# Kernel optimization log

Hardware: AMD Instinct MI355X
Metric: run time of the kernel (lower is better)

## Reference

```python
import jax, jax.numpy as jnp
import numpy as np

H = 4096
V = 32000
BT = 2048
IGNORE_INDEX = -100
WEIGHT_HARD = 0.5
WEIGHT_SOFT = 0.5
EPS = 1e-12  # F.normalize eps


def setup_inputs() -> dict:
    key = jax.random.key(0)
    k0, k1, k2, k3, k4 = jax.random.split(key, 5)
    student = jax.random.normal(k0, (BT, H // 2), dtype=jnp.float32)
    teacher = jax.random.normal(k1, (BT, H), dtype=jnp.float32)
    W_student = jax.random.normal(k2, (V, H // 2), dtype=jnp.float32) * (1.0 / np.sqrt(H // 2))
    W_teacher = jax.random.normal(k3, (V, H), dtype=jnp.float32) * (1.0 / np.sqrt(H))
    target = jax.random.randint(k4, (BT,), 0, V, dtype=jnp.int64)
    return {"student": student, "W_student": W_student, "teacher": teacher,
            "W_teacher": W_teacher, "target": target}


def reference(student, W_student, teacher, W_teacher, target):
    # Fused linear projections to vocab space
    s_logits = jnp.einsum("bh,vh->bv", student, W_student)   # [BT, V]
    t_logits = jnp.einsum("bh,vh->bv", teacher, W_teacher)   # [BT, V]

    n = target.shape[0]
    valid = target != IGNORE_INDEX                            # [BT]

    # Hard loss: cross-entropy(student_logits, target), sum over valid / BT
    logp = jax.nn.log_softmax(s_logits, axis=-1)
    safe_tgt = jnp.where(valid, target, 0)
    nll = -jnp.take_along_axis(logp, safe_tgt[:, None], axis=-1)[:, 0]
    hard_loss = jnp.sum(jnp.where(valid, nll, 0.0)) / n

    # Soft loss: 1 - cosine_similarity(student_logits, teacher_logits) per row
    s_norm = jnp.maximum(jnp.linalg.norm(s_logits, axis=-1, keepdims=True), EPS)
    t_norm = jnp.maximum(jnp.linalg.norm(t_logits, axis=-1, keepdims=True), EPS)
    cos = jnp.sum((s_logits / s_norm) * (t_logits / t_norm), axis=-1)  # [BT]
    soft_loss = jnp.sum(1.0 - cos) / n

    return WEIGHT_HARD * hard_loss + WEIGHT_SOFT * soft_loss
```

## Files before the change

kernel.cpp:

```cpp
#include <hip/hip_runtime.h>
#include <hip/hip_bf16.h>

#define H2 2048
#define HT 4096
#define NV 32000
#define NBT 2048

#define BM2 128
#define BN2 256
#define BK2 64
#define NVB2 (NV / BN2)

#define BM 128
#define BN 128
#define BK 32
#define LDT 40
#define NVB (NV / BN)

typedef __attribute__((ext_vector_type(8))) short short8;
typedef __attribute__((ext_vector_type(8))) unsigned short ushort8;
typedef __attribute__((ext_vector_type(4))) float floatx4;

static __device__ __forceinline__ unsigned int pk_bf16(float a, float b) {
  __hip_bfloat162 h = __float22bfloat162_rn(make_float2(a, b));
  union { __hip_bfloat162 h; unsigned int u; } c;
  c.h = h;
  return c.u;
}

static __device__ __forceinline__ void gload_lds16(const void* g, void* l) {
  __builtin_amdgcn_global_load_lds(
      (const __attribute__((address_space(1))) unsigned int*)g,
      (__attribute__((address_space(3))) unsigned int*)l, 16, 0, 0);
}

__global__ void cvt_bf16_kernel(const float* __restrict__ src,
                                unsigned int* __restrict__ dst, int n) {
  int i = blockIdx.x * blockDim.x + threadIdx.x;
  int base = i * 8;
  if (base >= n) return;
  float4 f0 = *(const float4*)(src + base);
  float4 f1 = *(const float4*)(src + base + 4);
  uint4 o;
  o.x = pk_bf16(f0.x, f0.y);
  o.y = pk_bf16(f0.z, f0.w);
  o.z = pk_bf16(f1.x, f1.y);
  o.w = pk_bf16(f1.z, f1.w);
  *(uint4*)(dst + i * 4) = o;
}


template <int K>
static __device__ __forceinline__ void gemm_pipe(
    const unsigned short* __restrict__ act,
    const unsigned short* __restrict__ w,
    const int row0, const int col0, const int tid,
    const int aoff, const int boff,
    unsigned short (*__restrict__ sA)[BM2 * BK2],
    unsigned short (*__restrict__ sB)[BN2 * BK2],
    floatx4 (&acc)[4][4])
{
  constexpr int NT = K / BK2;
  const int r8 = tid >> 3;
  const int usw = ((tid & 7) ^ (r8 & 7)) * 8;

  const unsigned short* pa0 = act + (size_t)(row0 + r8) * K + usw;
  const unsigned short* pa1 = pa0 + (size_t)64 * K;
  const unsigned short* pb0 = w + (size_t)(col0 + r8) * K + usw;
  const unsigned short* pb1 = pb0 + (size_t)64 * K;
  const unsigned short* pb2 = pb0 + (size_t)128 * K;
  const unsigned short* pb3 = pb0 + (size_t)192 * K;

#define STAGE6(buf)                                   \
  do {                                                \
    gload_lds16(pa0, &sA[buf][tid * 8]);              \
    gload_lds16(pa1, &sA[buf][4096 + tid * 8]);       \
    gload_lds16(pb0, &sB[buf][tid * 8]);              \
    gload_lds16(pb1, &sB[buf][4096 + tid * 8]);       \
    gload_lds16(pb2, &sB[buf][8192 + tid * 8]);       \
    gload_lds16(pb3, &sB[buf][12288 + tid * 8]);      \
    pa0 += BK2; pa1 += BK2;                           \
    pb0 += BK2; pb1 += BK2; pb2 += BK2; pb3 += BK2;   \
  } while (0)

  STAGE6(0);
  STAGE6(1);
  asm volatile("s_waitcnt vmcnt(6)" ::: "memory");
  __builtin_amdgcn_s_barrier();

#pragma unroll 1
  for (int t = 0; t < NT; ++t) {
    const int cur = t & 1;
    const unsigned short* sAc = sA[cur];
    const unsigned short* sBc = sB[cur];

    short8 a0[4], a1[4], b0[4], b1[4];
#pragma unroll
    for (int i = 0; i < 4; ++i) {
      a0[i] = *(const short8*)(sAc + (aoff + i * 1024));
      a1[i] = *(const short8*)(sAc + ((aoff ^ 32) + i * 1024));
    }
#pragma unroll
    for (int j = 0; j < 4; ++j) {
      b0[j] = *(const short8*)(sBc + (boff + j * 1024));
      b1[j] = *(const short8*)(sBc + ((boff ^ 32) + j * 1024));
    }
    asm volatile("s_waitcnt lgkmcnt(0)" ::: "memory");
    __builtin_amdgcn_s_barrier();

    if (t + 2 < NT) {
      STAGE6(cur);
      asm volatile("s_waitcnt vmcnt(6)" ::: "memory");
    } else if (t + 1 < NT) {
      asm volatile("s_waitcnt vmcnt(0)" ::: "memory");
    }
    __builtin_amdgcn_s_barrier();

    __builtin_amdgcn_s_setprio(1);
#pragma unroll
    for (int i = 0; i < 4; ++i)
#pragma unroll
      for (int j = 0; j < 4; ++j)
        acc[i][j] = __builtin_amdgcn_mfma_f32_16x16x32_bf16(
            a0[i], b0[j], acc[i][j], 0, 0, 0);
#pragma unroll
    for (int i = 0; i < 4; ++i)
#pragma unroll
      for (int j = 0; j < 4; ++j)
        acc[i][j] = __builtin_amdgcn_mfma_f32_16x16x32_bf16(
            a1[i], b1[j], acc[i][j], 0, 0, 0);
    __builtin_amdgcn_s_setprio(0);
  }
#undef STAGE6
}

__global__ __launch_bounds__(512, 2) void fused_gemm_pipe_kernel(
    const unsigned short* __restrict__ sbf,
    const unsigned short* __restrict__ tbf,
    const unsigned short* __restrict__ Wsb,
    const unsigned short* __restrict__ Wtb,
    const int* __restrict__ target,
    float* __restrict__ part,
    float* __restrict__ s_tgt_out)
{
  __shared__ unsigned short sA[2][BM2 * BK2];
  __shared__ unsigned short sB[2][BN2 * BK2];
  __shared__ float sRed[BM2][4];
  __shared__ int sTgt[BM2];

  const int tid = threadIdx.x;

  const int lin = blockIdx.x + (int)gridDim.x * blockIdx.y;
  const int swz = (lin & 7) * 250 + (lin >> 3);
  const int bx = swz & 15;
  const int by = swz >> 4;
  const int row0 = bx * BM2;
  const int col0 = by * BN2;

  if (tid < BM2) {
    sTgt[tid] = target[row0 + tid];
    sRed[tid][0] = 0.f; sRed[tid][1] = 0.f;
    sRed[tid][2] = 0.f; sRed[tid][3] = 0.f;
  }

  const int lane = tid & 63;
  const int wv = tid >> 6;
  const int wr = wv >> 2;
  const int wc = wv & 3;
  const int ku = lane >> 4;
  const int u0 = (ku ^ (lane & 7)) * 8;
  const int aoff = (wr * 64 + (lane & 15)) * BK2 + u0;
  const int boff = (wc * 64 + (lane & 15)) * BK2 + u0;

  floatx4 acc_s[4][4];
  floatx4 acc_t[4][4];
#pragma unroll
  for (int i = 0; i < 4; ++i)
#pragma unroll
    for (int j = 0; j < 4; ++j) {
      acc_s[i][j] = (floatx4){0.f, 0.f, 0.f, 0.f};
      acc_t[i][j] = (floatx4){0.f, 0.f, 0.f, 0.f};
    }

  gemm_pipe<H2>(sbf, Wsb, row0, col0, tid, aoff, boff, sA, sB, acc_s);
  gemm_pipe<HT>(tbf, Wtb, row0, col0, tid, aoff, boff, sA, sB, acc_t);

#pragma unroll
  for (int i = 0; i < 4; ++i) {
#pragma unroll
    for (int r = 0; r < 4; ++r) {
      const int row_l = wr * 64 + i * 16 + (lane >> 4) * 4 + r;
      float e = 0.f, dp = 0.f, ss = 0.f, tt = 0.f;
#pragma unroll
      for (int j = 0; j < 4; ++j) {
        float s = acc_s[i][j][r];
        float t = acc_t[i][j][r];
        e += __expf(s);
        dp += s * t;
        ss += s * s;
        tt += t * t;
        const int col_l = wc * 64 + j * 16 + (lane & 15);
        if (sTgt[row_l] == col0 + col_l) s_tgt_out[row0 + row_l] = s;
      }
#pragma unroll
      for (int off = 1; off < 16; off <<= 1) {
        e  += __shfl_xor(e,  off, 16);
        dp += __shfl_xor(dp, off, 16);
        ss += __shfl_xor(ss, off, 16);
        tt += __shfl_xor(tt, off, 16);
      }
      if ((lane & 15) == 0) {
        atomicAdd(&sRed[row_l][0], e);
        atomicAdd(&sRed[row_l][1], dp);
        atomicAdd(&sRed[row_l][2], ss);
        atomicAdd(&sRed[row_l][3], tt);
      }
    }
  }
  __syncthreads();
  if (tid < BM2) {
    float* p = part + (size_t)by * 4 * NBT + row0 + tid;
    p[0]       = sRed[tid][0];
    p[NBT]     = sRed[tid][1];
    p[2 * NBT] = sRed[tid][2];
    p[3 * NBT] = sRed[tid][3];
  }
}


__global__ __launch_bounds__(256, 2) void fused_gemm_kernel(
    const unsigned short* __restrict__ sbf,
    const unsigned short* __restrict__ tbf,
    const float* __restrict__ Ws,
    const float* __restrict__ Wt,
    const int* __restrict__ target,
    float* __restrict__ part,
    float* __restrict__ s_tgt_out)
{
  __shared__ unsigned short sA[BM * LDT];
  __shared__ unsigned short sB[BN * LDT];
  __shared__ float sRed[BM][4];
  __shared__ int sTgt[BM];

  const int tid = threadIdx.x;
  const int row0 = blockIdx.x * BM;
  const int col0 = blockIdx.y * BN;
  const int lane = tid & 63;
  const int wv = tid >> 6;
  const int wr = wv >> 1;
  const int wc = wv & 1;

  if (tid < BM) {
    sTgt[tid] = target[row0 + tid];
    sRed[tid][0] = 0.f; sRed[tid][1] = 0.f;
    sRed[tid][2] = 0.f; sRed[tid][3] = 0.f;
  }

  floatx4 acc_s[4][4];
  floatx4 acc_t[4][4];
#pragma unroll
  for (int i = 0; i < 4; ++i)
#pragma unroll
    for (int j = 0; j < 4; ++j) {
      acc_s[i][j] = (floatx4){0.f, 0.f, 0.f, 0.f};
      acc_t[i][j] = (floatx4){0.f, 0.f, 0.f, 0.f};
    }

  const int sr = tid >> 1;
  const int sk = (tid & 1) << 4;
  const int mrow = lane & 15;
  const int koff = (lane >> 4) << 3;
  const int abase = (wr * 64 + mrow) * LDT + koff;
  const int bbase = (wc * 64 + mrow) * LDT + koff;

  {
    const unsigned short* ap = sbf + (size_t)(row0 + sr) * H2 + sk;
    const float* bp = Ws + (size_t)(col0 + sr) * H2 + sk;
#pragma unroll 1
    for (int k0 = 0; k0 < H2; k0 += BK) {
      ushort8 a0 = *(const ushort8*)(ap);
      ushort8 a1 = *(const ushort8*)(ap + 8);
      float4 b0 = *(const float4*)(bp);
      float4 b1 = *(const float4*)(bp + 4);
      float4 b2 = *(const float4*)(bp + 8);
      float4 b3 = *(const float4*)(bp + 12);
      ap += BK; bp += BK;
      __syncthreads();
      *(ushort8*)(&sA[sr * LDT + sk]) = a0;
      *(ushort8*)(&sA[sr * LDT + sk + 8]) = a1;
      uint4 u0, u1;
      u0.x = pk_bf16(b0.x, b0.y); u0.y = pk_bf16(b0.z, b0.w);
      u0.z = pk_bf16(b1.x, b1.y); u0.w = pk_bf16(b1.z, b1.w);
      u1.x = pk_bf16(b2.x, b2.y); u1.y = pk_bf16(b2.z, b2.w);
      u1.z = pk_bf16(b3.x, b3.y); u1.w = pk_bf16(b3.z, b3.w);
      *(uint4*)(&sB[sr * LDT + sk]) = u0;
      *(uint4*)(&sB[sr * LDT + sk + 8]) = u1;
      __syncthreads();
      short8 af[4], bfrag[4];
#pragma unroll
      for (int i = 0; i < 4; ++i)
        af[i] = *(const short8*)(&sA[abase + i * 16 * LDT]);
#pragma unroll
      for (int j = 0; j < 4; ++j)
        bfrag[j] = *(const short8*)(&sB[bbase + j * 16 * LDT]);
#pragma unroll
      for (int i = 0; i < 4; ++i)
#pragma unroll
        for (int j = 0; j < 4; ++j)
          acc_s[i][j] = __builtin_amdgcn_mfma_f32_16x16x32_bf16(
              af[i], bfrag[j], acc_s[i][j], 0, 0, 0);
    }
  }
  {
    const unsigned short* ap = tbf + (size_t)(row0 + sr) * HT + sk;
    const float* bp = Wt + (size_t)(col0 + sr) * HT + sk;
#pragma unroll 1
    for (int k0 = 0; k0 < HT; k0 += BK) {
      ushort8 a0 = *(const ushort8*)(ap);
      ushort8 a1 = *(const ushort8*)(ap + 8);
      float4 b0 = *(const float4*)(bp);
      float4 b1 = *(const float4*)(bp + 4);
      float4 b2 = *(const float4*)(bp + 8);
      float4 b3 = *(const float4*)(bp + 12);
      ap += BK; bp += BK;
      __syncthreads();
      *(ushort8*)(&sA[sr * LDT + sk]) = a0;
      *(ushort8*)(&sA[sr * LDT + sk + 8]) = a1;
      uint4 u0, u1;
      u0.x = pk_bf16(b0.x, b0.y); u0.y = pk_bf16(b0.z, b0.w);
      u0.z = pk_bf16(b1.x, b1.y); u0.w = pk_bf16(b1.z, b1.w);
      u1.x = pk_bf16(b2.x, b2.y); u1.y = pk_bf16(b2.z, b2.w);
      u1.z = pk_bf16(b3.x, b3.y); u1.w = pk_bf16(b3.z, b3.w);
      *(uint4*)(&sB[sr * LDT + sk]) = u0;
      *(uint4*)(&sB[sr * LDT + sk + 8]) = u1;
      __syncthreads();
      short8 af[4], bfrag[4];
#pragma unroll
      for (int i = 0; i < 4; ++i)
        af[i] = *(const short8*)(&sA[abase + i * 16 * LDT]);
#pragma unroll
      for (int j = 0; j < 4; ++j)
        bfrag[j] = *(const short8*)(&sB[bbase + j * 16 * LDT]);
#pragma unroll
      for (int i = 0; i < 4; ++i)
#pragma unroll
        for (int j = 0; j < 4; ++j)
          acc_t[i][j] = __builtin_amdgcn_mfma_f32_16x16x32_bf16(
              af[i], bfrag[j], acc_t[i][j], 0, 0, 0);
    }
  }

#pragma unroll
  for (int i = 0; i < 4; ++i) {
#pragma unroll
    for (int r = 0; r < 4; ++r) {
      const int row_l = wr * 64 + i * 16 + (lane >> 4) * 4 + r;
      float e = 0.f, dp = 0.f, ss = 0.f, tt = 0.f;
#pragma unroll
      for (int j = 0; j < 4; ++j) {
        float s = acc_s[i][j][r];
        float t = acc_t[i][j][r];
        e += __expf(s);
        dp += s * t;
        ss += s * s;
        tt += t * t;
        const int col_l = wc * 64 + j * 16 + (lane & 15);
        if (sTgt[row_l] == col0 + col_l) s_tgt_out[row0 + row_l] = s;
      }
#pragma unroll
      for (int off = 1; off < 16; off <<= 1) {
        e  += __shfl_xor(e,  off, 16);
        dp += __shfl_xor(dp, off, 16);
        ss += __shfl_xor(ss, off, 16);
        tt += __shfl_xor(tt, off, 16);
      }
      if ((lane & 15) == 0) {
        atomicAdd(&sRed[row_l][0], e);
        atomicAdd(&sRed[row_l][1], dp);
        atomicAdd(&sRed[row_l][2], ss);
        atomicAdd(&sRed[row_l][3], tt);
      }
    }
  }
  __syncthreads();
  if (tid < BM) {
    float* p = part + (size_t)blockIdx.y * 4 * NBT + row0 + tid;
    p[0]       = sRed[tid][0];
    p[NBT]     = sRed[tid][1];
    p[2 * NBT] = sRed[tid][2];
    p[3 * NBT] = sRed[tid][3];
  }
}


__global__ void row_loss_kernel(const float* __restrict__ part,
                                const float* __restrict__ s_tgt,
                                const int* __restrict__ target,
                                float* __restrict__ row_loss, int nvb) {
  const int row = blockIdx.x * blockDim.x + threadIdx.x;
  if (row >= NBT) return;
  float e = 0.f, dp = 0.f, ss = 0.f, tt = 0.f;
  for (int v = 0; v < nvb; ++v) {
    const float* p = part + (size_t)v * 4 * NBT + row;
    e  += p[0];
    dp += p[NBT];
    ss += p[2 * NBT];
    tt += p[3 * NBT];
  }
  const float lse = logf(e);
  const int tg = target[row];
  const float st = s_tgt[row];
  const float nll = (tg != -100) ? (lse - st) : 0.f;
  const float ns = fmaxf(sqrtf(ss), 1e-12f);
  const float nt = fmaxf(sqrtf(tt), 1e-12f);
  const float c = dp / (ns * nt);
  row_loss[row] = (0.5f * nll + 0.5f * (1.f - c)) * (1.f / (float)NBT);
}

__global__ void final_reduce_kernel(const float* __restrict__ row_loss,
                                    float* __restrict__ out) {
  __shared__ float sm[4];
  float v = 0.f;
  for (int i = threadIdx.x; i < NBT; i += 256) v += row_loss[i];
#pragma unroll
  for (int off = 32; off >= 1; off >>= 1) v += __shfl_down(v, off, 64);
  if ((threadIdx.x & 63) == 0) sm[threadIdx.x >> 6] = v;
  __syncthreads();
  if (threadIdx.x == 0) out[0] = sm[0] + sm[1] + sm[2] + sm[3];
}

extern "C" void kernel_launch(void* const* d_in, const int* in_sizes, int n_in,
                              void* d_out, int out_size, void* d_ws, size_t ws_size,
                              hipStream_t stream) {
  const float* student = (const float*)d_in[0];
  const float* Ws      = (const float*)d_in[1];
  const float* teacher = (const float*)d_in[2];
  const float* Wt      = (const float*)d_in[3];
  const int*   target  = (const int*)d_in[4];

  const size_t nS  = (size_t)NBT * H2;
  const size_t nT  = (size_t)NBT * HT;
  const size_t nWs = (size_t)NV * H2;
  const size_t nWt = (size_t)NV * HT;
  const size_t nPart2 = (size_t)NVB2 * 4 * NBT;
  const size_t nPart  = (size_t)NVB * 4 * NBT;

  const size_t ws_needed_big =
      (nS + nT + nWs + nWt) * 2 + (nPart2 + 2 * NBT) * 4;

  if (ws_size >= ws_needed_big) {
    unsigned short* sbf = (unsigned short*)d_ws;
    unsigned short* tbf = sbf + nS;
    unsigned short* Wsb = tbf + nT;
    unsigned short* Wtb = Wsb + nWs;
    float* part     = (float*)(Wtb + nWt);
    float* s_tgt    = part + nPart2;
    float* row_loss = s_tgt + NBT;

    cvt_bf16_kernel<<<(int)(nS / 8 / 256), 256, 0, stream>>>(
        student, (unsigned int*)sbf, (int)nS);
    cvt_bf16_kernel<<<(int)(nT / 8 / 256), 256, 0, stream>>>(
        teacher, (unsigned int*)tbf, (int)nT);
    cvt_bf16_kernel<<<(int)(nWs / 8 / 256), 256, 0, stream>>>(
        Ws, (unsigned int*)Wsb, (int)nWs);
    cvt_bf16_kernel<<<(int)(nWt / 8 / 256), 256, 0, stream>>>(
        Wt, (unsigned int*)Wtb, (int)nWt);

    dim3 grid(NBT / BM2, NV / BN2);
    fused_gemm_pipe_kernel<<<grid, 512, 0, stream>>>(
        sbf, tbf, Wsb, Wtb, target, part, s_tgt);

    row_loss_kernel<<<NBT / 256, 256, 0, stream>>>(part, s_tgt, target,
                                                   row_loss, NVB2);
    final_reduce_kernel<<<1, 256, 0, stream>>>(row_loss, (float*)d_out);
  } else {
    unsigned short* sbf = (unsigned short*)d_ws;
    unsigned short* tbf = sbf + nS;
    float* part     = (float*)(tbf + nT);
    float* s_tgt    = part + nPart;
    float* row_loss = s_tgt + NBT;

    cvt_bf16_kernel<<<(int)(nS / 8 / 256), 256, 0, stream>>>(
        student, (unsigned int*)sbf, (int)nS);
    cvt_bf16_kernel<<<(int)(nT / 8 / 256), 256, 0, stream>>>(
        teacher, (unsigned int*)tbf, (int)nT);

    dim3 grid(NBT / BM, NV / BN);
    fused_gemm_kernel<<<grid, 256, 0, stream>>>(sbf, tbf, Ws, Wt, target,
                                                part, s_tgt);

    row_loss_kernel<<<NBT / 256, 256, 0, stream>>>(part, s_tgt, target,
                                                   row_loss, NVB);
    final_reduce_kernel<<<1, 256, 0, stream>>>(row_loss, (float*)d_out);
  }
}
```

Measured before the change: 1.986 ms.

## Triple-buffer GEMM LDS pipeline, merge bf16 conversions, wave-parallel row loss

The pipelined GEMM moves from double to triple LDS buffering. Loads for stage t+2 are issued before reading stage t, so one barrier pair per iteration covers the global-to-LDS latency. Launch bounds drop to one block per SM because the shared memory footprint grows. The four bf16 conversion launches are merged into one grid-stride kernel, and row_loss now has each 64-lane wave reduce one row's partials with shuffles instead of a serial loop per thread. The risk is that lower occupancy could offset the deeper pipeline.

```diff
diff --git a/kernel.cpp b/kernel.cpp
--- a/kernel.cpp
+++ b/kernel.cpp
@@ -49,6 +49,36 @@
   *(uint4*)(dst + i * 4) = o;
 }
 
+__global__ void cvt_all_kernel(const float* __restrict__ s0,
+                               const float* __restrict__ s1,
+                               const float* __restrict__ s2,
+                               const float* __restrict__ s3,
+                               unsigned int* __restrict__ d0,
+                               unsigned int* __restrict__ d1,
+                               unsigned int* __restrict__ d2,
+                               unsigned int* __restrict__ d3,
+                               int c0, int c1, int c2, int c3) {
+  for (int g = blockIdx.x * blockDim.x + threadIdx.x; g < c3;
+       g += gridDim.x * blockDim.x) {
+    const float* src;
+    unsigned int* dst;
+    int l;
+    if (g < c0)      { src = s0; dst = d0; l = g; }
+    else if (g < c1) { src = s1; dst = d1; l = g - c0; }
+    else if (g < c2) { src = s2; dst = d2; l = g - c1; }
+    else             { src = s3; dst = d3; l = g - c2; }
+    const float* p = src + (size_t)l * 8;
+    float4 f0 = *(const float4*)(p);
+    float4 f1 = *(const float4*)(p + 4);
+    uint4 o;
+    o.x = pk_bf16(f0.x, f0.y);
+    o.y = pk_bf16(f0.z, f0.w);
+    o.z = pk_bf16(f1.x, f1.y);
+    o.w = pk_bf16(f1.z, f1.w);
+    *(uint4*)(dst + (size_t)l * 4) = o;
+  }
+}
+
 
 template <int K>
 static __device__ __forceinline__ void gemm_pipe(
@@ -83,18 +113,31 @@
     pb0 += BK2; pb1 += BK2; pb2 += BK2; pb3 += BK2;   \
   } while (0)
 
+  asm volatile("s_waitcnt lgkmcnt(0)" ::: "memory");
+  __builtin_amdgcn_s_barrier();
   STAGE6(0);
   STAGE6(1);
-  asm volatile("s_waitcnt vmcnt(6)" ::: "memory");
-  __builtin_amdgcn_s_barrier();
-
+
+  int bc = 0;
+  int bs = 2;
 #pragma unroll 1
   for (int t = 0; t < NT; ++t) {
-    const int cur = t & 1;
-    const unsigned short* sAc = sA[cur];
-    const unsigned short* sBc = sB[cur];
-
-    short8 a0[4], a1[4], b0[4], b1[4];
+    asm volatile("s_waitcnt lgkmcnt(0)" ::: "memory");
+    __builtin_amdgcn_s_barrier();
+
+    if (t + 2 < NT) {
+      STAGE6(bs);
+      asm volatile("s_waitcnt vmcnt(12)" ::: "memory");
+    } else if (t + 1 < NT) {
+      asm volatile("s_waitcnt vmcnt(6)" ::: "memory");
+    } else {
+      asm volatile("s_waitcnt vmcnt(0)" ::: "memory");
+    }
+    __builtin_amdgcn_s_barrier();
+
+    const unsigned short* sAc = sA[bc];
+    const unsigned short* sBc = sB[bc];
+    short8 a0[4], a1[4], b0v[4], b1v[4];
 #pragma unroll
     for (int i = 0; i < 4; ++i) {
       a0[i] = *(const short8*)(sAc + (aoff + i * 1024));
@@ -102,19 +145,9 @@
     }
 #pragma unroll
     for (int j = 0; j < 4; ++j) {
-      b0[j] = *(const short8*)(sBc + (boff + j * 1024));
-      b1[j] = *(const short8*)(sBc + ((boff ^ 32) + j * 1024));
-    }
-    asm volatile("s_waitcnt lgkmcnt(0)" ::: "memory");
-    __builtin_amdgcn_s_barrier();
-
-    if (t + 2 < NT) {
-      STAGE6(cur);
-      asm volatile("s_waitcnt vmcnt(6)" ::: "memory");
-    } else if (t + 1 < NT) {
-      asm volatile("s_waitcnt vmcnt(0)" ::: "memory");
-    }
-    __builtin_amdgcn_s_barrier();
+      b0v[j] = *(const short8*)(sBc + (boff + j * 1024));
+      b1v[j] = *(const short8*)(sBc + ((boff ^ 32) + j * 1024));
+    }
 
     __builtin_amdgcn_s_setprio(1);
 #pragma unroll
@@ -122,19 +155,22 @@
 #pragma unroll
       for (int j = 0; j < 4; ++j)
         acc[i][j] = __builtin_amdgcn_mfma_f32_16x16x32_bf16(
-            a0[i], b0[j], acc[i][j], 0, 0, 0);
+            a0[i], b0v[j], acc[i][j], 0, 0, 0);
 #pragma unroll
     for (int i = 0; i < 4; ++i)
 #pragma unroll
       for (int j = 0; j < 4; ++j)
         acc[i][j] = __builtin_amdgcn_mfma_f32_16x16x32_bf16(
-            a1[i], b1[j], acc[i][j], 0, 0, 0);
+            a1[i], b1v[j], acc[i][j], 0, 0, 0);
     __builtin_amdgcn_s_setprio(0);
+
+    bc = (bc == 2) ? 0 : bc + 1;
+    bs = (bs == 2) ? 0 : bs + 1;
   }
 #undef STAGE6
 }
 
-__global__ __launch_bounds__(512, 2) void fused_gemm_pipe_kernel(
+__global__ __launch_bounds__(512, 1) void fused_gemm_pipe_kernel(
     const unsigned short* __restrict__ sbf,
     const unsigned short* __restrict__ tbf,
     const unsigned short* __restrict__ Wsb,
@@ -143,8 +179,8 @@
     float* __restrict__ part,
     float* __restrict__ s_tgt_out)
 {
-  __shared__ unsigned short sA[2][BM2 * BK2];
-  __shared__ unsigned short sB[2][BN2 * BK2];
+  __shared__ unsigned short sA[3][BM2 * BK2];
+  __shared__ unsigned short sB[3][BN2 * BK2];
   __shared__ float sRed[BM2][4];
   __shared__ int sTgt[BM2];
 
@@ -397,24 +433,34 @@
                                 const float* __restrict__ s_tgt,
                                 const int* __restrict__ target,
                                 float* __restrict__ row_loss, int nvb) {
-  const int row = blockIdx.x * blockDim.x + threadIdx.x;
+  const int lane = threadIdx.x & 63;
+  const int row = blockIdx.x * (blockDim.x >> 6) + (threadIdx.x >> 6);
   if (row >= NBT) return;
   float e = 0.f, dp = 0.f, ss = 0.f, tt = 0.f;
-  for (int v = 0; v < nvb; ++v) {
+  for (int v = lane; v < nvb; v += 64) {
     const float* p = part + (size_t)v * 4 * NBT + row;
     e  += p[0];
     dp += p[NBT];
     ss += p[2 * NBT];
     tt += p[3 * NBT];
   }
-  const float lse = logf(e);
-  const int tg = target[row];
-  const float st = s_tgt[row];
-  const float nll = (tg != -100) ? (lse - st) : 0.f;
-  const float ns = fmaxf(sqrtf(ss), 1e-12f);
-  const float nt = fmaxf(sqrtf(tt), 1e-12f);
-  const float c = dp / (ns * nt);
-  row_loss[row] = (0.5f * nll + 0.5f * (1.f - c)) * (1.f / (float)NBT);
+#pragma unroll
+  for (int off = 32; off >= 1; off >>= 1) {
+    e  += __shfl_xor(e,  off, 64);
+    dp += __shfl_xor(dp, off, 64);
+    ss += __shfl_xor(ss, off, 64);
+    tt += __shfl_xor(tt, off, 64);
+  }
+  if (lane == 0) {
+    const float lse = logf(e);
+    const int tg = target[row];
+    const float st = s_tgt[row];
+    const float nll = (tg != -100) ? (lse - st) : 0.f;
+    const float ns = fmaxf(sqrtf(ss), 1e-12f);
+    const float nt = fmaxf(sqrtf(tt), 1e-12f);
+    const float c = dp / (ns * nt);
+    row_loss[row] = (0.5f * nll + 0.5f * (1.f - c)) * (1.f / (float)NBT);
+  }
 }
 
 __global__ void final_reduce_kernel(const float* __restrict__ row_loss,
@@ -457,21 +503,22 @@
     float* s_tgt    = part + nPart2;
     float* row_loss = s_tgt + NBT;
 
-    cvt_bf16_kernel<<<(int)(nS / 8 / 256), 256, 0, stream>>>(
-        student, (unsigned int*)sbf, (int)nS);
-    cvt_bf16_kernel<<<(int)(nT / 8 / 256), 256, 0, stream>>>(
-        teacher, (unsigned int*)tbf, (int)nT);
-    cvt_bf16_kernel<<<(int)(nWs / 8 / 256), 256, 0, stream>>>(
-        Ws, (unsigned int*)Wsb, (int)nWs);
-    cvt_bf16_kernel<<<(int)(nWt / 8 / 256), 256, 0, stream>>>(
-        Wt, (unsigned int*)Wtb, (int)nWt);
+    const int c0 = (int)(nS / 8);
+    const int c1 = c0 + (int)(nT / 8);
+    const int c2 = c1 + (int)(nWs / 8);
+    const int c3 = c2 + (int)(nWt / 8);
+    cvt_all_kernel<<<2048, 256, 0, stream>>>(
+        student, teacher, Ws, Wt,
+        (unsigned int*)sbf, (unsigned int*)tbf,
+        (unsigned int*)Wsb, (unsigned int*)Wtb,
+        c0, c1, c2, c3);
 
     dim3 grid(NBT / BM2, NV / BN2);
     fused_gemm_pipe_kernel<<<grid, 512, 0, stream>>>(
         sbf, tbf, Wsb, Wtb, target, part, s_tgt);
 
-    row_loss_kernel<<<NBT / 256, 256, 0, stream>>>(part, s_tgt, target,
-                                                   row_loss, NVB2);
+    row_loss_kernel<<<NBT / 4, 256, 0, stream>>>(part, s_tgt, target,
+                                                 row_loss, NVB2);
     final_reduce_kernel<<<1, 256, 0, stream>>>(row_loss, (float*)d_out);
   } else {
     unsigned short* sbf = (unsigned short*)d_ws;
@@ -489,8 +536,8 @@
     fused_gemm_kernel<<<grid, 256, 0, stream>>>(sbf, tbf, Ws, Wt, target,
                                                 part, s_tgt);
 
-    row_loss_kernel<<<NBT / 256, 256, 0, stream>>>(part, s_tgt, target,
-                                                   row_loss, NVB);
+    row_loss_kernel<<<NBT / 4, 256, 0, stream>>>(part, s_tgt, target,
+                                                 row_loss, NVB);
     final_reduce_kernel<<<1, 256, 0, stream>>>(row_loss, (float*)d_out);
   }
 }
```

Measured after the change: 2.163 ms. +8.9%, slower.
